# Kernel optimization log

Hardware: AMD Instinct MI355X
Metric: run time of the kernel (lower is better)

## Reference

```python
import jax, jax.numpy as jnp
import numpy as np

V = 10000        # one-hot depth per sparse feature
N_DENSE = 13
N_SPARSE = 26
FIELD = N_DENSE + N_SPARSE       # 39
K = 8
FEAT = N_DENSE + N_SPARSE * V    # 260013
BATCH = 4096


def setup_inputs() -> dict:
    key = jax.random.key(0)
    k1, k2, k3, k4 = jax.random.split(key, 4)
    dense = jax.random.normal(k1, (BATCH, N_DENSE), dtype=jnp.float32)
    sparse = jax.random.randint(k2, (BATCH, N_SPARSE), 0, V)
    w0 = jnp.zeros((1,), dtype=jnp.float32)
    w = jax.random.normal(k3, (FEAT, 1), dtype=jnp.float32) * 0.05
    v = jax.random.normal(k4, (FEAT, FIELD, K), dtype=jnp.float32) * 0.05
    return {"dense": dense, "sparse": sparse, "w0": w0, "w": w, "v": v}


def reference(dense, sparse, w0, w, v):
    # Row offsets of each sparse feature's one-hot block inside the
    # concatenated feature vector x = [dense(13) | onehot_0(V) | ... | onehot_25(V)].
    offsets = N_DENSE + jnp.arange(N_SPARSE) * V          # [26]
    idx = sparse.astype(jnp.int32) + offsets[None, :]     # [B, 26] flat feature ids

    # linear_part = x @ w + w0  (one-hot matmul == gather)
    linear = dense @ w[:N_DENSE] \
        + jnp.sum(w[idx, 0], axis=1, keepdims=True) + w0  # [B, 1]

    # field_f = tensordot(x, v, axes=1): dense contribution + gathered rows
    field_f = jnp.einsum('bd,dfk->bfk', dense, v[:N_DENSE]) \
        + jnp.sum(v[idx], axis=1)                         # [B, FIELD, K]

    # sum_{i<j} <f_i, f_j> = 0.5 * (||sum_i f_i||^2 - sum_i ||f_i||^2)
    S = jnp.sum(field_f, axis=1)                          # [B, K]
    inter = 0.5 * (jnp.sum(S * S, axis=1)
                   - jnp.sum(field_f * field_f, axis=(1, 2)))  # [B]

    return linear + inter[:, None]                        # [B, 1]
```

## Files before the change

kernel.cpp:

```cpp
#include <hip/hip_runtime.h>


constexpr int V_DEPTH  = 10000;
constexpr int N_DENSE  = 13;
constexpr int N_SPARSE = 26;
constexpr int FIELD    = 39;
constexpr int K        = 8;
constexpr int FK       = FIELD * K;
constexpr int BLOCK    = 320;
constexpr int NWAVES   = BLOCK / 64;

__global__ __launch_bounds__(BLOCK) void ffm_fwd_kernel(
    const float* __restrict__ dense,
    const int*   __restrict__ sparse,
    const float* __restrict__ w0,
    const float* __restrict__ w,
    const float* __restrict__ v,
    float*       __restrict__ out)
{
    const int b = blockIdx.x;
    const int t = threadIdx.x;

    __shared__ float s_dense[N_DENSE];
    __shared__ int   s_idx[N_SPARSE];
    __shared__ float s_wg[N_SPARSE];
    __shared__ float s_sq[NWAVES];
    __shared__ float s_Sk[NWAVES][K];

    if (t < N_DENSE) s_dense[t] = dense[b * N_DENSE + t];
    if (t < N_SPARSE) {
        const int id = sparse[b * N_SPARSE + t] + N_DENSE + t * V_DEPTH;
        s_idx[t] = id;
        s_wg[t]  = w[id];
    }
    __syncthreads();

    float acc = 0.0f;
    if (t < FK) {
        #pragma unroll
        for (int d = 0; d < N_DENSE; ++d)
            acc += s_dense[d] * v[d * FK + t];
        #pragma unroll
        for (int j = 0; j < N_SPARSE; ++j)
            acc += v[(size_t)s_idx[j] * FK + t];
    }

    float sq = acc * acc;
    float sk = acc;
    #pragma unroll
    for (int off = 32; off >= 1; off >>= 1)
        sq += __shfl_xor(sq, off, 64);
    #pragma unroll
    for (int off = 32; off >= 8; off >>= 1)
        sk += __shfl_xor(sk, off, 64);

    const int wave = t >> 6;
    const int lane = t & 63;
    if (lane == 0) s_sq[wave] = sq;
    if (lane < K)  s_Sk[wave][lane] = sk;
    __syncthreads();

    if (t == 0) {
        float sumsq = 0.0f;
        #pragma unroll
        for (int wv = 0; wv < NWAVES; ++wv) sumsq += s_sq[wv];

        float ssum = 0.0f;
        #pragma unroll
        for (int k = 0; k < K; ++k) {
            float Sk = 0.0f;
            #pragma unroll
            for (int wv = 0; wv < NWAVES; ++wv) Sk += s_Sk[wv][k];
            ssum += Sk * Sk;
        }

        float linear = w0[0];
        #pragma unroll
        for (int j = 0; j < N_SPARSE; ++j) linear += s_wg[j];
        #pragma unroll
        for (int d = 0; d < N_DENSE; ++d)  linear += s_dense[d] * w[d];

        out[b] = linear + 0.5f * (ssum - sumsq);
    }
}

extern "C" void kernel_launch(void* const* d_in, const int* in_sizes, int n_in,
                              void* d_out, int out_size, void* d_ws, size_t ws_size,
                              hipStream_t stream) {
    const float* dense  = (const float*)d_in[0];
    const int*   sparse = (const int*)  d_in[1];
    const float* w0     = (const float*)d_in[2];
    const float* w      = (const float*)d_in[3];
    const float* v      = (const float*)d_in[4];
    float* out = (float*)d_out;

    const int batch = out_size;
    ffm_fwd_kernel<<<batch, BLOCK, 0, stream>>>(dense, sparse, w0, w, v, out);
}
```

Before: 391.3 us.

## Vectorize v gathers to float4 and process four batch rows per block

```diff
diff --git a/kernel.cpp b/kernel.cpp
--- a/kernel.cpp
+++ b/kernel.cpp
@@ -7,8 +7,11 @@
 constexpr int FIELD    = 39;
 constexpr int K        = 8;
 constexpr int FK       = FIELD * K;
-constexpr int BLOCK    = 320;
-constexpr int NWAVES   = BLOCK / 64;
+constexpr int SLOT     = FK / 4;
+constexpr int SLOTP    = 80;
+constexpr int RPB      = 4;
+constexpr int BLOCK    = RPB * SLOTP;
+constexpr int NGRP     = SLOTP / 16;
 
 __global__ __launch_bounds__(BLOCK) void ffm_fwd_kernel(
     const float* __restrict__ dense,
@@ -16,71 +19,110 @@
     const float* __restrict__ w0,
     const float* __restrict__ w,
     const float* __restrict__ v,
-    float*       __restrict__ out)
+    float*       __restrict__ out,
+    int batch)
 {
-    const int b = blockIdx.x;
-    const int t = threadIdx.x;
+    const int b0 = blockIdx.x * RPB;
+    const int t  = threadIdx.x;
 
-    __shared__ float s_dense[N_DENSE];
-    __shared__ int   s_idx[N_SPARSE];
-    __shared__ float s_wg[N_SPARSE];
-    __shared__ float s_sq[NWAVES];
-    __shared__ float s_Sk[NWAVES][K];
+    __shared__ int   s_idx[RPB][N_SPARSE];
+    __shared__ float s_wg[RPB][N_SPARSE];
+    __shared__ float s_dense[RPB][N_DENSE];
+    __shared__ float s_wd[N_DENSE];
+    __shared__ float s_S[RPB][NGRP][2][4];
+    __shared__ float s_sq[RPB][NGRP];
 
-    if (t < N_DENSE) s_dense[t] = dense[b * N_DENSE + t];
-    if (t < N_SPARSE) {
-        const int id = sparse[b * N_SPARSE + t] + N_DENSE + t * V_DEPTH;
-        s_idx[t] = id;
-        s_wg[t]  = w[id];
+    if (t < RPB * N_SPARSE) {
+        const int r = t / N_SPARSE, j = t - r * N_SPARSE;
+        const int row = b0 + r;
+        int id = N_DENSE;
+        float wg = 0.0f;
+        if (row < batch) {
+            id = sparse[row * N_SPARSE + j] + N_DENSE + j * V_DEPTH;
+            wg = w[id];
+        }
+        s_idx[r][j] = id;
+        s_wg[r][j]  = wg;
+    } else if (t >= 128 && t < 128 + RPB * N_DENSE) {
+        const int u = t - 128;
+        const int r = u / N_DENSE, d = u - r * N_DENSE;
+        const int row = b0 + r;
+        s_dense[r][d] = (row < batch) ? dense[row * N_DENSE + d] : 0.0f;
+    } else if (t >= 192 && t < 192 + N_DENSE) {
+        s_wd[t - 192] = w[t - 192];
     }
     __syncthreads();
 
-    float acc = 0.0f;
-    if (t < FK) {
+    const int r = t / SLOTP;
+    const int s = t - r * SLOTP;
+
+    float ax = 0.0f, ay = 0.0f, az = 0.0f, aw = 0.0f;
+    if (s < SLOT) {
+        const float4* __restrict__ v4 = reinterpret_cast<const float4*>(v);
         #pragma unroll
-        for (int d = 0; d < N_DENSE; ++d)
-            acc += s_dense[d] * v[d * FK + t];
+        for (int d = 0; d < N_DENSE; ++d) {
+            const float4 g = v4[d * SLOT + s];
+            const float sd = s_dense[r][d];
+            ax = fmaf(sd, g.x, ax); ay = fmaf(sd, g.y, ay);
+            az = fmaf(sd, g.z, az); aw = fmaf(sd, g.w, aw);
+        }
         #pragma unroll
-        for (int j = 0; j < N_SPARSE; ++j)
-            acc += v[(size_t)s_idx[j] * FK + t];
+        for (int j = 0; j < N_SPARSE; ++j) {
+            const float4 g = v4[s_idx[r][j] * SLOT + s];
+            ax += g.x; ay += g.y; az += g.z; aw += g.w;
+        }
     }
 
-    float sq = acc * acc;
-    float sk = acc;
+    float sq = ax * ax + ay * ay + az * az + aw * aw;
     #pragma unroll
-    for (int off = 32; off >= 1; off >>= 1)
-        sq += __shfl_xor(sq, off, 64);
+    for (int off = 8; off >= 1; off >>= 1) sq += __shfl_xor(sq, off, 64);
+
+    float sx = ax, sy = ay, sz = az, sw = aw;
     #pragma unroll
-    for (int off = 32; off >= 8; off >>= 1)
-        sk += __shfl_xor(sk, off, 64);
+    for (int off = 8; off >= 2; off >>= 1) {
+        sx += __shfl_xor(sx, off, 64);
+        sy += __shfl_xor(sy, off, 64);
+        sz += __shfl_xor(sz, off, 64);
+        sw += __shfl_xor(sw, off, 64);
+    }
 
-    const int wave = t >> 6;
-    const int lane = t & 63;
-    if (lane == 0) s_sq[wave] = sq;
-    if (lane < K)  s_Sk[wave][lane] = sk;
+    const int grp = s >> 4;
+    const int sl  = s & 15;
+    if (sl < 2) {
+        s_S[r][grp][sl][0] = sx;
+        s_S[r][grp][sl][1] = sy;
+        s_S[r][grp][sl][2] = sz;
+        s_S[r][grp][sl][3] = sw;
+        if (sl == 0) s_sq[r][grp] = sq;
+    }
     __syncthreads();
 
-    if (t == 0) {
+    if (t < RPB && (b0 + t) < batch) {
+        const int rr = t;
+        float S[K];
+        #pragma unroll
+        for (int k = 0; k < K; ++k) S[k] = 0.0f;
         float sumsq = 0.0f;
         #pragma unroll
-        for (int wv = 0; wv < NWAVES; ++wv) sumsq += s_sq[wv];
-
+        for (int g = 0; g < NGRP; ++g) {
+            #pragma unroll
+            for (int i = 0; i < 4; ++i) {
+                S[i]     += s_S[rr][g][0][i];
+                S[4 + i] += s_S[rr][g][1][i];
+            }
+            sumsq += s_sq[rr][g];
+        }
         float ssum = 0.0f;
         #pragma unroll
-        for (int k = 0; k < K; ++k) {
-            float Sk = 0.0f;
-            #pragma unroll
-            for (int wv = 0; wv < NWAVES; ++wv) Sk += s_Sk[wv][k];
-            ssum += Sk * Sk;
-        }
+        for (int k = 0; k < K; ++k) ssum += S[k] * S[k];
 
         float linear = w0[0];
         #pragma unroll
-        for (int j = 0; j < N_SPARSE; ++j) linear += s_wg[j];
+        for (int j = 0; j < N_SPARSE; ++j) linear += s_wg[rr][j];
         #pragma unroll
-        for (int d = 0; d < N_DENSE; ++d)  linear += s_dense[d] * w[d];
+        for (int d = 0; d < N_DENSE; ++d)  linear += s_dense[rr][d] * s_wd[d];
 
-        out[b] = linear + 0.5f * (ssum - sumsq);
+        out[b0 + rr] = linear + 0.5f * (ssum - sumsq);
     }
 }
 
@@ -95,5 +137,6 @@
     float* out = (float*)d_out;
 
     const int batch = out_size;
-    ffm_fwd_kernel<<<batch, BLOCK, 0, stream>>>(dense, sparse, w0, w, v, out);
+    const int grid  = (batch + RPB - 1) / RPB;
+    ffm_fwd_kernel<<<grid, BLOCK, 0, stream>>>(dense, sparse, w0, w, v, out, batch);
 }
```

New measurement: 389.1 us. Within noise of the previous version (-0.6%).
